# Kernel tuning notes

Hardware: AMD Instinct MI355X
Metric: run time of the kernel (lower is better)

## Reference

```python
import jax, jax.numpy as jnp
import numpy as np

NUM_GROUPS = 32
EPS = 1e-5


def setup_inputs() -> dict:
    key = jax.random.key(0)
    ks = jax.random.split(key, 6)
    B, C, H, W = 8, 128, 64, 64
    d = C // 8
    x = jax.random.normal(ks[0], (B, C, H, W), dtype=jnp.float32)
    # conv 1x1 weights stored as [out_ch, in_ch]; scaled like torch kaiming-uniform-ish
    s = 1.0 / np.sqrt(C)
    return {
        "x": x,
        "gn_w": jnp.ones((C,), jnp.float32),
        "gn_b": jnp.zeros((C,), jnp.float32),
        "q_w": jax.random.normal(ks[1], (d, C), jnp.float32) * s,
        "q_b": jnp.zeros((d,), jnp.float32),
        "k_w": jax.random.normal(ks[2], (d, C), jnp.float32) * s,
        "k_b": jnp.zeros((d,), jnp.float32),
        "v_w": jax.random.normal(ks[3], (C, C), jnp.float32) * s,
        "v_b": jnp.zeros((C,), jnp.float32),
        "p_w": jax.random.normal(ks[4], (C, C), jnp.float32) * s,
        "p_b": jnp.zeros((C,), jnp.float32),
    }


def _group_norm(x, w, b):
    B, C, H, W = x.shape
    g = NUM_GROUPS
    xr = x.reshape(B, g, C // g, H, W)
    mu = xr.mean(axis=(2, 3, 4), keepdims=True)
    var = xr.var(axis=(2, 3, 4), keepdims=True)
    xn = ((xr - mu) * jax.lax.rsqrt(var + EPS)).reshape(B, C, H, W)
    return xn * w[None, :, None, None] + b[None, :, None, None]


def reference(x, gn_w, gn_b, q_w, q_b, k_w, k_b, v_w, v_b, p_w, p_b):
    B, C, H, W = x.shape
    N = H * W
    h_ = _group_norm(x, gn_w, gn_b)            # [B,C,H,W]
    hf = h_.reshape(B, C, N)                   # flatten spatial
    # 1x1 convs == channel matmuls
    q = jnp.einsum('dc,bcn->bnd', q_w, hf) + q_b[None, None, :]   # [B,N,d]
    k = jnp.einsum('dc,bcn->bnd', k_w, hf) + k_b[None, None, :]   # [B,N,d]
    v = jnp.einsum('ec,bcn->ben', v_w, hf) + v_b[None, :, None]   # [B,C,N]
    d = q.shape[-1]
    scale = jnp.asarray(int(d) ** (-0.5), x.dtype)
    attn = jnp.einsum('bid,bjd->bij', q, k) * scale               # [B,N,N]
    attn = jax.nn.softmax(attn, axis=-1)
    a = jnp.einsum('bcj,bij->bci', v, attn)                       # [B,C,N]
    proj = jnp.einsum('ec,bcn->ben', p_w, a) + p_b[None, :, None]
    return x + proj.reshape(B, C, H, W)
```

## Files before the change

kernel.cpp:

```cpp
#include <hip/hip_runtime.h>
#include <math.h>


typedef short v8s __attribute__((ext_vector_type(8)));
typedef float v16f __attribute__((ext_vector_type(16)));

__device__ __forceinline__ unsigned short f2bf_rne(float f) {
  unsigned u = __float_as_uint(f);
  u += 0x7fffu + ((u >> 16) & 1u);
  return (unsigned short)(u >> 16);
}

__device__ __forceinline__ v8s mk8(unsigned a, unsigned b, unsigned c, unsigned d) {
  union { unsigned u[4]; v8s s; } x;
  x.u[0] = a; x.u[1] = b; x.u[2] = c; x.u[3] = d;
  return x.s;
}

__device__ __forceinline__ unsigned pack_trunc(float hi, float lo) {
  return __builtin_amdgcn_perm(__float_as_uint(hi), __float_as_uint(lo), 0x07060302u);
}

#define VT(b, n, c) (((((size_t)(b) * 256 + ((n) >> 4)) << 7) + (c)) * 16 + ((n) & 15))

#define WSB_MURS   0u
#define WSB_WCATB  4096u
#define WSB_BCAT   49152u
#define WSB_PWB    65536u
#define WSB_QBF    131072u
#define WSB_KBF    1310720u
#define WSB_VBF    2621440u
#define WSB_ABF    11534336u

__global__ void prep_kernel(const float* __restrict__ qw, const float* __restrict__ qb,
                            const float* __restrict__ kw, const float* __restrict__ kb,
                            const float* __restrict__ vw, const float* __restrict__ vb,
                            const float* __restrict__ pw,
                            unsigned short* __restrict__ wcatb, float* __restrict__ bcat,
                            unsigned short* __restrict__ pwb) {
  const float qs = 0.36067376022224085f;
  int idx = blockIdx.x * 256 + threadIdx.x;
  if (idx < 160 * 128) {
    int o = idx >> 7, c = idx & 127;
    float val;
    if (o < 16)       val = qw[o * 128 + c] * qs;
    else if (o < 32)  val = kw[(o - 16) * 128 + c];
    else              val = vw[(o - 32) * 128 + c];
    wcatb[idx] = f2bf_rne(val);
  } else if (idx < 160 * 128 + 160) {
    int o = idx - 160 * 128;
    bcat[o] = (o < 16) ? qb[o] * qs : (o < 32) ? kb[o - 16] : vb[o - 32];
  } else if (idx < 160 * 128 + 160 + 128 * 128) {
    int j = idx - (160 * 128 + 160);
    pwb[j] = f2bf_rne(pw[j]);
  }
}

__global__ __launch_bounds__(512)
void gn_stats_kernel(const float* __restrict__ x, float* __restrict__ mu_rs) {
  const int id = blockIdx.x;
  const int bg = (id & 7) * 32 + (id >> 3);
  const float4* xp = (const float4*)(x + (size_t)bg * 16384);
  float s = 0.f, ss = 0.f;
#pragma unroll
  for (int u = 0; u < 8; ++u) {
    int i = threadIdx.x + u * 512;
    float4 v = xp[i];
    s  += v.x + v.y + v.z + v.w;
    ss += v.x * v.x + v.y * v.y + v.z * v.z + v.w * v.w;
  }
  for (int off = 32; off > 0; off >>= 1) {
    s  += __shfl_down(s, off, 64);
    ss += __shfl_down(ss, off, 64);
  }
  __shared__ float red[16];
  int lane = threadIdx.x & 63, wid = threadIdx.x >> 6;
  if (lane == 0) { red[wid * 2] = s; red[wid * 2 + 1] = ss; }
  __syncthreads();
  if (threadIdx.x == 0) {
    float S = 0.f, SS = 0.f;
    for (int w = 0; w < 8; ++w) { S += red[w * 2]; SS += red[w * 2 + 1]; }
    float mu  = S * (1.0f / 16384.0f);
    float var = SS * (1.0f / 16384.0f) - mu * mu;
    float rs  = rsqrtf(var + 1e-5f);
    mu_rs[bg * 2]     = mu;
    mu_rs[bg * 2 + 1] = rs;
  }
}

__global__ __launch_bounds__(512)
void qkv_kernel(const float* __restrict__ x, const float* __restrict__ gnw,
                const float* __restrict__ gnb, const float* __restrict__ mu_rs,
                const unsigned short* __restrict__ wcatb, const float* __restrict__ bcat,
                unsigned short* __restrict__ qbf, unsigned short* __restrict__ kbf,
                unsigned short* __restrict__ vbf) {
  __shared__ float scs[128], shs[128], bsh[160];
  const int id = blockIdx.x;
  const int b = id & 7, nb = (id >> 3) << 6;
  const int t = threadIdx.x;
  const int w = t >> 6, lane = t & 63, h = lane >> 5, l = lane & 31;
  const int nsub = w & 1, og = w >> 1;
  if (t < 128) {
    float mu = mu_rs[(b * 32 + (t >> 2)) * 2];
    float rs = mu_rs[(b * 32 + (t >> 2)) * 2 + 1];
    float gw = gnw[t], gb = gnb[t];
    scs[t] = rs * gw; shs[t] = gb - mu * rs * gw;
  }
  if (t < 160) bsh[t] = bcat[t];
  __syncthreads();

  const int n = nb + nsub * 32 + l;
  const float* xb = x + ((size_t)b * 128 << 12);
  const int otbase = (og == 0) ? 0 : og + 1;

  float xv[64];
#pragma unroll
  for (int ks = 0; ks < 8; ++ks)
#pragma unroll
    for (int p = 0; p < 8; ++p)
      xv[ks * 8 + p] = xb[((size_t)(ks * 16 + 8 * h + p) << 12) + n];

  v16f acc[2];
#pragma unroll
  for (int a2 = 0; a2 < 2; ++a2)
#pragma unroll
    for (int r = 0; r < 16; ++r) acc[a2][r] = 0.f;

#pragma unroll
  for (int ks = 0; ks < 8; ++ks) {
    const int c0 = ks * 16 + 8 * h;
    unsigned fd[4];
#pragma unroll
    for (int p = 0; p < 4; ++p) {
      int ca = c0 + 2 * p;
      float h0 = xv[ks * 8 + 2 * p]     * scs[ca]     + shs[ca];
      float h1 = xv[ks * 8 + 2 * p + 1] * scs[ca + 1] + shs[ca + 1];
      fd[p] = (unsigned)f2bf_rne(h0) | ((unsigned)f2bf_rne(h1) << 16);
    }
    v8s bf = mk8(fd[0], fd[1], fd[2], fd[3]);
    {
      v8s af = *(const v8s*)(wcatb + (otbase * 32 + l) * 128 + ks * 16 + 8 * h);
      acc[0] = __builtin_amdgcn_mfma_f32_32x32x16_bf16(af, bf, acc[0], 0, 0, 0);
    }
    if (og == 0) {
      v8s af = *(const v8s*)(wcatb + (32 + l) * 128 + ks * 16 + 8 * h);
      acc[1] = __builtin_amdgcn_mfma_f32_32x32x16_bf16(af, bf, acc[1], 0, 0, 0);
    }
  }

  if (og == 0) {
    const size_t nqk = ((size_t)b * 4096 + n) << 4;
#pragma unroll
    for (int r = 0; r < 16; ++r) {
      int o = 4 * h + (r & 3) + 8 * (r >> 2);
      unsigned short bv = f2bf_rne(acc[0][r] + bsh[o]);
      if (o < 16) qbf[nqk + o] = bv; else kbf[nqk + o - 16] = bv;
    }
#pragma unroll
    for (int r = 0; r < 16; ++r) {
      int o = 32 + 4 * h + (r & 3) + 8 * (r >> 2);
      vbf[VT(b, n, o - 32)] = f2bf_rne(acc[1][r] + bsh[o]);
    }
  } else {
#pragma unroll
    for (int r = 0; r < 16; ++r) {
      int o = otbase * 32 + 4 * h + (r & 3) + 8 * (r >> 2);
      vbf[VT(b, n, o - 32)] = f2bf_rne(acc[0][r] + bsh[o]);
    }
  }
}

#define VS 40

__global__ __launch_bounds__(512)
void attn_kernel(const unsigned short* __restrict__ qbf,
                 const unsigned short* __restrict__ kbf,
                 const unsigned short* __restrict__ vbf,
                 unsigned short* __restrict__ abf) {
  __shared__ alignas(16) unsigned char smemb[65536];
  __shared__ float l_lds[128];
  unsigned short* const vlds = (unsigned short*)smemb;
  float* const comb = (float*)smemb;

  const int id = blockIdx.x;
  const int b = id & 7, i0 = (id >> 3) << 7;
  const int t = threadIdx.x;
  const int w = t >> 6, lane = t & 63, h = lane >> 5, l = lane & 31;
  const int jsub = w & 1, iquad = w >> 1;

  const unsigned short* kg = kbf + ((size_t)b << 16);
  const unsigned short* vg = vbf + ((size_t)b << 19);

  const v8s qf = *(const v8s*)(qbf + (((size_t)(b * 4096 + i0 + iquad * 32 + l)) << 4) + 8 * h);

  v16f zc;
#pragma unroll
  for (int r = 0; r < 16; ++r) zc[r] = 0.f;
  v16f acc[4];
#pragma unroll
  for (int ct = 0; ct < 4; ++ct)
#pragma unroll
    for (int r = 0; r < 16; ++r) acc[ct][r] = 0.f;
  float ls = 0.f;

  const int vrow = w * 64 + (lane >> 1);
  const int sh16 = (lane & 1) * 8;

  if (t < 128) l_lds[t] = 0.f;

  for (int tile = 0; tile < 64; ++tile) {
    v8s s0 = *(const v8s*)(vg + (size_t)tile * 8192 + vrow * 16 + sh16);
    v8s s1 = *(const v8s*)(vg + (size_t)tile * 8192 + (vrow + 32) * 16 + sh16);
    v8s kf = *(const v8s*)(kg + (((size_t)(tile * 64 + jsub * 32 + l)) << 4) + 8 * h);

    __syncthreads();

    *(v8s*)(vlds + vrow * VS + sh16) = s0;
    *(v8s*)(vlds + (vrow + 32) * VS + sh16) = s1;

    v16f st = __builtin_amdgcn_mfma_f32_32x32x16_bf16(kf, qf, zc, 0, 0, 0);
    float pe[16];
#pragma unroll
    for (int r = 0; r < 16; ++r) { pe[r] = __builtin_amdgcn_exp2f(st[r]); ls += pe[r]; }
    unsigned G[8];
#pragma unroll
    for (int g = 0; g < 4; ++g) {
      G[2 * g]     = pack_trunc(pe[4 * g + 1], pe[4 * g]);
      G[2 * g + 1] = pack_trunc(pe[4 * g + 3], pe[4 * g + 2]);
    }
    unsigned S0 = h ? G[0] : G[2], S1 = h ? G[1] : G[3];
    unsigned S2 = h ? G[4] : G[6], S3 = h ? G[5] : G[7];
    unsigned R0 = (unsigned)__shfl_xor((int)S0, 32, 64);
    unsigned R1 = (unsigned)__shfl_xor((int)S1, 32, 64);
    unsigned R2 = (unsigned)__shfl_xor((int)S2, 32, 64);
    unsigned R3 = (unsigned)__shfl_xor((int)S3, 32, 64);
    v8s pf0 = h ? mk8(R0, R1, G[2], G[3]) : mk8(G[0], G[1], R0, R1);
    v8s pf1 = h ? mk8(R2, R3, G[6], G[7]) : mk8(G[4], G[5], R2, R3);

    __syncthreads();

#pragma unroll
    for (int ct = 0; ct < 4; ++ct) {
      v8s vf0 = *(const v8s*)(vlds + ((jsub * 2) * 128 + ct * 32 + l) * VS + 8 * h);
      v8s vf1 = *(const v8s*)(vlds + ((jsub * 2 + 1) * 128 + ct * 32 + l) * VS + 8 * h);
      acc[ct] = __builtin_amdgcn_mfma_f32_32x32x16_bf16(vf0, pf0, acc[ct], 0, 0, 0);
      acc[ct] = __builtin_amdgcn_mfma_f32_32x32x16_bf16(vf1, pf1, acc[ct], 0, 0, 0);
    }
  }

  atomicAdd(&l_lds[iquad * 32 + l], ls);
  __syncthreads();

  float* const myreg = comb + iquad * 4096;
  if (jsub == 1) {
#pragma unroll
    for (int ct = 0; ct < 4; ++ct)
#pragma unroll
      for (int q = 0; q < 4; ++q) {
        float4 v4 = {acc[ct][4 * q], acc[ct][4 * q + 1],
                     acc[ct][4 * q + 2], acc[ct][4 * q + 3]};
        *(float4*)&myreg[ct * 1024 + lane * 16 + 4 * q] = v4;
      }
  }
  __syncthreads();
  if (jsub == 0) {
    const float li = 1.f / l_lds[iquad * 32 + l];
#pragma unroll
    for (int ct = 0; ct < 4; ++ct) {
#pragma unroll
      for (int q = 0; q < 4; ++q) {
        float4 v4 = *(float4*)&myreg[ct * 1024 + lane * 16 + 4 * q];
        acc[ct][4 * q]     += v4.x;
        acc[ct][4 * q + 1] += v4.y;
        acc[ct][4 * q + 2] += v4.z;
        acc[ct][4 * q + 3] += v4.w;
      }
#pragma unroll
      for (int r = 0; r < 16; ++r) {
        int c = ct * 32 + 4 * h + (r & 3) + 8 * (r >> 2);
        abf[((size_t)(b * 128 + c) << 12) + i0 + iquad * 32 + l] =
            f2bf_rne(acc[ct][r] * li);
      }
    }
  }
}

__global__ __launch_bounds__(512)
void proj_kernel(const unsigned short* __restrict__ abf, const unsigned short* __restrict__ pwb,
                 const float* __restrict__ pb, const float* __restrict__ x,
                 float* __restrict__ out) {
  __shared__ float pbs[128];
  const int id = blockIdx.x;
  const int b = id & 7, nb = (id >> 3) << 6;
  const int t = threadIdx.x;
  const int w = t >> 6, lane = t & 63, h = lane >> 5, l = lane & 31;
  const int nsub = w & 1, ot = w >> 1;
  if (t < 128) pbs[t] = pb[t];
  __syncthreads();

  const int n = nb + nsub * 32 + l;
  const unsigned short* ab = abf + (((size_t)b * 128) << 12);

  unsigned short av[64];
#pragma unroll
  for (int ks = 0; ks < 8; ++ks)
#pragma unroll
    for (int p = 0; p < 8; ++p)
      av[ks * 8 + p] = ab[((size_t)(ks * 16 + 8 * h + p) << 12) + n];

  v16f acc;
#pragma unroll
  for (int r = 0; r < 16; ++r) acc[r] = 0.f;

#pragma unroll
  for (int ks = 0; ks < 8; ++ks) {
    unsigned fd[4];
#pragma unroll
    for (int p = 0; p < 4; ++p)
      fd[p] = (unsigned)av[ks * 8 + 2 * p] | ((unsigned)av[ks * 8 + 2 * p + 1] << 16);
    v8s bf = mk8(fd[0], fd[1], fd[2], fd[3]);
    v8s af = *(const v8s*)(pwb + (ot * 32 + l) * 128 + ks * 16 + 8 * h);
    acc = __builtin_amdgcn_mfma_f32_32x32x16_bf16(af, bf, acc, 0, 0, 0);
  }

#pragma unroll
  for (int r = 0; r < 16; ++r) {
    int e = ot * 32 + 4 * h + (r & 3) + 8 * (r >> 2);
    size_t idx = ((size_t)(b * 128 + e) << 12) + n;
    out[idx] = acc[r] + pbs[e] + x[idx];
  }
}

extern "C" void kernel_launch(void* const* d_in, const int* in_sizes, int n_in,
                              void* d_out, int out_size, void* d_ws, size_t ws_size,
                              hipStream_t stream) {
  const float* x   = (const float*)d_in[0];
  const float* gnw = (const float*)d_in[1];
  const float* gnb = (const float*)d_in[2];
  const float* qw  = (const float*)d_in[3];
  const float* qb  = (const float*)d_in[4];
  const float* kw  = (const float*)d_in[5];
  const float* kb  = (const float*)d_in[6];
  const float* vw  = (const float*)d_in[7];
  const float* vb  = (const float*)d_in[8];
  const float* pw  = (const float*)d_in[9];
  const float* pb  = (const float*)d_in[10];
  float* out = (float*)d_out;
  char* ws = (char*)d_ws;

  float* mu_rs = (float*)(ws + WSB_MURS);
  unsigned short* wcatb = (unsigned short*)(ws + WSB_WCATB);
  float* bcat = (float*)(ws + WSB_BCAT);
  unsigned short* pwb = (unsigned short*)(ws + WSB_PWB);
  unsigned short* qbf = (unsigned short*)(ws + WSB_QBF);
  unsigned short* kbf = (unsigned short*)(ws + WSB_KBF);
  unsigned short* vbf = (unsigned short*)(ws + WSB_VBF);
  unsigned short* abf = (unsigned short*)(ws + WSB_ABF);

  hipLaunchKernelGGL(prep_kernel, dim3(145), dim3(256), 0, stream,
                     qw, qb, kw, kb, vw, vb, pw, wcatb, bcat, pwb);
  hipLaunchKernelGGL(gn_stats_kernel, dim3(256), dim3(512), 0, stream, x, mu_rs);
  hipLaunchKernelGGL(qkv_kernel, dim3(512), dim3(512), 0, stream,
                     x, gnw, gnb, mu_rs, wcatb, bcat, qbf, kbf, vbf);
  hipLaunchKernelGGL(attn_kernel, dim3(256), dim3(512), 0, stream,
                     qbf, kbf, vbf, abf);
  hipLaunchKernelGGL(proj_kernel, dim3(512), dim3(512), 0, stream,
                     abf, pwb, pb, x, out);
}
```

Before: 171.0 us.

## Double-buffer V tiles in attention with smaller blocks and transposed Q layout

The attention kernel now uses 256-thread blocks covering 64 queries each, launched as 512 blocks, and double-buffers the V tile in LDS. The next tile's global loads are issued before the current tile's MFMAs, so each iteration needs one barrier instead of two. Q is stored channel-major by the QKV kernel, which makes its writes coalesced but turns the attention kernel's Q fragment load into scattered 2-byte gathers. Each block loads the full V stream for only half as many queries, so global V traffic doubles. In exchange, occupancy and latency hiding should improve.

```diff
diff --git a/kernel.cpp b/kernel.cpp
--- a/kernel.cpp
+++ b/kernel.cpp
@@ -92,7 +92,7 @@
 void qkv_kernel(const float* __restrict__ x, const float* __restrict__ gnw,
                 const float* __restrict__ gnb, const float* __restrict__ mu_rs,
                 const unsigned short* __restrict__ wcatb, const float* __restrict__ bcat,
-                unsigned short* __restrict__ qbf, unsigned short* __restrict__ kbf,
+                unsigned short* __restrict__ qTb, unsigned short* __restrict__ kbf,
                 unsigned short* __restrict__ vbf) {
   __shared__ float scs[128], shs[128], bsh[160];
   const int id = blockIdx.x;
@@ -154,7 +154,8 @@
     for (int r = 0; r < 16; ++r) {
       int o = 4 * h + (r & 3) + 8 * (r >> 2);
       unsigned short bv = f2bf_rne(acc[0][r] + bsh[o]);
-      if (o < 16) qbf[nqk + o] = bv; else kbf[nqk + o - 16] = bv;
+      if (o < 16) qTb[((size_t)(b * 16 + o) << 12) + n] = bv;
+      else        kbf[nqk + o - 16] = bv;
     }
 #pragma unroll
     for (int r = 0; r < 16; ++r) {
@@ -170,28 +171,34 @@
   }
 }
 
-#define VS 40
-
-__global__ __launch_bounds__(512)
-void attn_kernel(const unsigned short* __restrict__ qbf,
+#define VS 24
+
+__global__ __launch_bounds__(256)
+void attn_kernel(const unsigned short* __restrict__ qTb,
                  const unsigned short* __restrict__ kbf,
                  const unsigned short* __restrict__ vbf,
                  unsigned short* __restrict__ abf) {
-  __shared__ alignas(16) unsigned char smemb[65536];
-  __shared__ float l_lds[128];
-  unsigned short* const vlds = (unsigned short*)smemb;
-  float* const comb = (float*)smemb;
+  __shared__ alignas(16) unsigned short smem[2][512 * VS];
+  __shared__ float l_lds[64];
 
   const int id = blockIdx.x;
-  const int b = id & 7, i0 = (id >> 3) << 7;
+  const int b = id & 7, i0 = (id >> 3) << 6;
   const int t = threadIdx.x;
   const int w = t >> 6, lane = t & 63, h = lane >> 5, l = lane & 31;
-  const int jsub = w & 1, iquad = w >> 1;
+  const int jsub = w & 1, ihalf = w >> 1;
 
   const unsigned short* kg = kbf + ((size_t)b << 16);
   const unsigned short* vg = vbf + ((size_t)b << 19);
 
-  const v8s qf = *(const v8s*)(qbf + (((size_t)(b * 4096 + i0 + iquad * 32 + l)) << 4) + 8 * h);
+  const int iglob = i0 + ihalf * 32 + l;
+  unsigned qd[4];
+#pragma unroll
+  for (int e = 0; e < 4; ++e) {
+    unsigned lo = qTb[((size_t)(b * 16 + 8 * h + 2 * e) << 12) + iglob];
+    unsigned hi = qTb[((size_t)(b * 16 + 8 * h + 2 * e + 1) << 12) + iglob];
+    qd[e] = lo | (hi << 16);
+  }
+  const v8s qf = mk8(qd[0], qd[1], qd[2], qd[3]);
 
   v16f zc;
 #pragma unroll
@@ -203,20 +210,28 @@
     for (int r = 0; r < 16; ++r) acc[ct][r] = 0.f;
   float ls = 0.f;
 
-  const int vrow = w * 64 + (lane >> 1);
+  const int srow = w * 128 + (lane >> 1);
   const int sh16 = (lane & 1) * 8;
 
-  if (t < 128) l_lds[t] = 0.f;
+#pragma unroll
+  for (int u = 0; u < 4; ++u) {
+    v8s a = *(const v8s*)(vg + (size_t)(srow + 32 * u) * 16 + sh16);
+    *(v8s*)(&smem[0][(srow + 32 * u) * VS + sh16]) = a;
+  }
+  if (t < 64) l_lds[t] = 0.f;
+  __syncthreads();
 
   for (int tile = 0; tile < 64; ++tile) {
-    v8s s0 = *(const v8s*)(vg + (size_t)tile * 8192 + vrow * 16 + sh16);
-    v8s s1 = *(const v8s*)(vg + (size_t)tile * 8192 + (vrow + 32) * 16 + sh16);
+    const int tn = (tile + 1) & 63;
+    unsigned short* const cur = smem[tile & 1];
+    unsigned short* const nxt = smem[(tile + 1) & 1];
+
+    v8s s[4];
+#pragma unroll
+    for (int u = 0; u < 4; ++u)
+      s[u] = *(const v8s*)(vg + (size_t)tn * 8192 + (size_t)(srow + 32 * u) * 16 + sh16);
+
     v8s kf = *(const v8s*)(kg + (((size_t)(tile * 64 + jsub * 32 + l)) << 4) + 8 * h);
-
-    __syncthreads();
-
-    *(v8s*)(vlds + vrow * VS + sh16) = s0;
-    *(v8s*)(vlds + (vrow + 32) * VS + sh16) = s1;
 
     v16f st = __builtin_amdgcn_mfma_f32_32x32x16_bf16(kf, qf, zc, 0, 0, 0);
     float pe[16];
@@ -237,21 +252,25 @@
     v8s pf0 = h ? mk8(R0, R1, G[2], G[3]) : mk8(G[0], G[1], R0, R1);
     v8s pf1 = h ? mk8(R2, R3, G[6], G[7]) : mk8(G[4], G[5], R2, R3);
 
-    __syncthreads();
-
 #pragma unroll
     for (int ct = 0; ct < 4; ++ct) {
-      v8s vf0 = *(const v8s*)(vlds + ((jsub * 2) * 128 + ct * 32 + l) * VS + 8 * h);
-      v8s vf1 = *(const v8s*)(vlds + ((jsub * 2 + 1) * 128 + ct * 32 + l) * VS + 8 * h);
+      v8s vf0 = *(const v8s*)(&cur[((jsub * 2) * 128 + ct * 32 + l) * VS + 8 * h]);
+      v8s vf1 = *(const v8s*)(&cur[((jsub * 2 + 1) * 128 + ct * 32 + l) * VS + 8 * h]);
       acc[ct] = __builtin_amdgcn_mfma_f32_32x32x16_bf16(vf0, pf0, acc[ct], 0, 0, 0);
       acc[ct] = __builtin_amdgcn_mfma_f32_32x32x16_bf16(vf1, pf1, acc[ct], 0, 0, 0);
     }
-  }
-
-  atomicAdd(&l_lds[iquad * 32 + l], ls);
-  __syncthreads();
-
-  float* const myreg = comb + iquad * 4096;
+
+#pragma unroll
+    for (int u = 0; u < 4; ++u)
+      *(v8s*)(&nxt[(srow + 32 * u) * VS + sh16]) = s[u];
+
+    __syncthreads();
+  }
+
+  atomicAdd(&l_lds[ihalf * 32 + l], ls);
+  __syncthreads();
+
+  float* const ov = (float*)smem;
   if (jsub == 1) {
 #pragma unroll
     for (int ct = 0; ct < 4; ++ct)
@@ -259,17 +278,17 @@
       for (int q = 0; q < 4; ++q) {
         float4 v4 = {acc[ct][4 * q], acc[ct][4 * q + 1],
                      acc[ct][4 * q + 2], acc[ct][4 * q + 3]};
-        *(float4*)&myreg[ct * 1024 + lane * 16 + 4 * q] = v4;
+        *(float4*)&ov[((ct * 2 + ihalf) * 32 + l) * 36 + 4 * h + 8 * q] = v4;
       }
   }
   __syncthreads();
   if (jsub == 0) {
-    const float li = 1.f / l_lds[iquad * 32 + l];
+    const float li = 1.f / l_lds[ihalf * 32 + l];
 #pragma unroll
     for (int ct = 0; ct < 4; ++ct) {
 #pragma unroll
       for (int q = 0; q < 4; ++q) {
-        float4 v4 = *(float4*)&myreg[ct * 1024 + lane * 16 + 4 * q];
+        float4 v4 = *(float4*)&ov[((ct * 2 + ihalf) * 32 + l) * 36 + 4 * h + 8 * q];
         acc[ct][4 * q]     += v4.x;
         acc[ct][4 * q + 1] += v4.y;
         acc[ct][4 * q + 2] += v4.z;
@@ -278,7 +297,7 @@
 #pragma unroll
       for (int r = 0; r < 16; ++r) {
         int c = ct * 32 + 4 * h + (r & 3) + 8 * (r >> 2);
-        abf[((size_t)(b * 128 + c) << 12) + i0 + iquad * 32 + l] =
+        abf[((size_t)(b * 128 + c) << 12) + (size_t)(i0 + ihalf * 32 + l)] =
             f2bf_rne(acc[ct][r] * li);
       }
     }
@@ -352,7 +371,7 @@
   unsigned short* wcatb = (unsigned short*)(ws + WSB_WCATB);
   float* bcat = (float*)(ws + WSB_BCAT);
   unsigned short* pwb = (unsigned short*)(ws + WSB_PWB);
-  unsigned short* qbf = (unsigned short*)(ws + WSB_QBF);
+  unsigned short* qTb = (unsigned short*)(ws + WSB_QBF);
   unsigned short* kbf = (unsigned short*)(ws + WSB_KBF);
   unsigned short* vbf = (unsigned short*)(ws + WSB_VBF);
   unsigned short* abf = (unsigned short*)(ws + WSB_ABF);
@@ -361,9 +380,9 @@
                      qw, qb, kw, kb, vw, vb, pw, wcatb, bcat, pwb);
   hipLaunchKernelGGL(gn_stats_kernel, dim3(256), dim3(512), 0, stream, x, mu_rs);
   hipLaunchKernelGGL(qkv_kernel, dim3(512), dim3(512), 0, stream,
-                     x, gnw, gnb, mu_rs, wcatb, bcat, qbf, kbf, vbf);
-  hipLaunchKernelGGL(attn_kernel, dim3(256), dim3(512), 0, stream,
-                     qbf, kbf, vbf, abf);
+                     x, gnw, gnb, mu_rs, wcatb, bcat, qTb, kbf, vbf);
+  hipLaunchKernelGGL(attn_kernel, dim3(512), dim3(256), 0, stream,
+                     qTb, kbf, vbf, abf);
   hipLaunchKernelGGL(proj_kernel, dim3(512), dim3(512), 0, stream,
                      abf, pwb, pb, x, out);
 }
```

New measurement: 166.8 us. 1.02x faster.
